# Performance work log

Measured on AMD Instinct MI355X. Metric: run time of the kernel, lower is better.

Reference implementation:

```python
import jax, jax.numpy as jnp
import numpy as np

N, FEAT, NCLS = 8192, 1024, 64


def setup_inputs() -> dict:
    key = jax.random.key(0)
    k1, k2, k3, k4, k5, k6 = jax.random.split(key, 6)
    x = jax.random.normal(k1, (N, FEAT), dtype=jnp.float32)
    adj = jax.random.uniform(k2, (N, N), dtype=jnp.float32)  # pairwise distances
    stdv1 = 1.0 / np.sqrt(FEAT)
    W1 = jax.random.uniform(k3, (FEAT, FEAT), jnp.float32, -stdv1, stdv1)
    b1 = jax.random.uniform(k4, (FEAT,), jnp.float32, -stdv1, stdv1)
    W2 = jax.random.uniform(k5, (FEAT, NCLS), jnp.float32, -stdv1, stdv1)
    b2 = jax.random.uniform(k6, (NCLS,), jnp.float32, -stdv1, stdv1)
    alpha = jnp.full((1,), 0.3, dtype=jnp.float32)
    return {"x": x, "adj": adj, "W1": W1, "b1": b1, "W2": W2, "b2": b2,
            "alpha": alpha, "K": 32}


def reference(x, adj, W1, b1, W2, b2, alpha, K):
    # --- top-K smallest-distance neighbor selection per row ---
    neg_vals, idx = jax.lax.top_k(-adj, K)        # K smallest adj entries per row
    vals = -neg_vals                              # [N, K] distances
    w = jnp.exp(-alpha[0] * vals)                 # 1 / exp(alpha * d)
    w = w / jnp.sum(w, axis=1, keepdims=True)     # row-normalize edge weights

    def spmm(h):
        # sparse A @ h using top-K edge list: out[i] = sum_k w[i,k] * h[idx[i,k]]
        return jnp.einsum('nk,nkf->nf', w, h[idx])

    # 2-layer GCN path of SimTSC (eval mode: dropout is identity)
    h = jax.nn.relu(spmm(x @ W1) + b1)            # [N, FEAT]
    out = spmm(h @ W2) + b2                       # [N, NCLS]
    return jax.nn.log_softmax(out, axis=1)
```

## Files before the change

### kernel.cpp

```cpp
#include <hip/hip_runtime.h>

typedef __bf16 bf16_t;
typedef __bf16 bf16x4 __attribute__((ext_vector_type(4)));
typedef __bf16 bf16x8 __attribute__((ext_vector_type(8)));
typedef float  f32x4  __attribute__((ext_vector_type(4)));

typedef const __attribute__((address_space(1))) void gvoid_t;
typedef __attribute__((address_space(3))) void lvoid_t;

#define N_NODES 8192
#define FEAT    1024
#define NCLS    64
#define TK      32

__device__ __forceinline__ float wave_min_f32(float v) {
  int x = __float_as_int(v), t;
#define STEPF(ctrl) t = __builtin_amdgcn_update_dpp(x, x, ctrl, 0xf, 0xf, false); \
                    v = fminf(v, __int_as_float(t)); x = __float_as_int(v);
  STEPF(0x111)
  STEPF(0x112)
  STEPF(0x114)
  STEPF(0x118)
  STEPF(0x142)
  STEPF(0x143)
#undef STEPF
  return __int_as_float(__builtin_amdgcn_readlane(x, 63));
}

__device__ __forceinline__ unsigned wave_min_u32(unsigned v) {
  int x = (int)v, t;
#define STEPU(ctrl) t = __builtin_amdgcn_update_dpp(x, x, ctrl, 0xf, 0xf, false); \
                    x = (int)((unsigned)x < (unsigned)t ? (unsigned)x : (unsigned)t);
  STEPU(0x111)
  STEPU(0x112)
  STEPU(0x114)
  STEPU(0x118)
  STEPU(0x142)
  STEPU(0x143)
#undef STEPU
  return (unsigned)__builtin_amdgcn_readlane(x, 63);
}

__global__ __launch_bounds__(256) void topk_kernel(const float* __restrict__ adj,
                                                   const float* __restrict__ alphap,
                                                   const float* __restrict__ x,
                                                   bf16_t* __restrict__ x_bf,
                                                   int* __restrict__ idx_out,
                                                   float* __restrict__ w_out,
                                                   const float* __restrict__ W1,
                                                   bf16_t* __restrict__ W1t,
                                                   const float* __restrict__ W2,
                                                   bf16_t* __restrict__ W2t) {
  const int tid = threadIdx.x;
  __shared__ float tile[64][65];
  __shared__ float svals[256];
  __shared__ int   sidx[256];
  __shared__ int   scnt;

  if (blockIdx.x >= N_NODES) {
    const int tb = blockIdx.x - N_NODES;
    const int bxi = tb % 17, by = tb / 17;
    const float* in;
    bf16_t* out;
    int cols, bx;
    if (bxi < 16) { in = W1; out = W1t; cols = FEAT; bx = bxi; }
    else          { in = W2; out = W2t; cols = NCLS; bx = 0; }
#pragma unroll
    for (int i = 0; i < 16; ++i) {
      int li = i * 256 + tid;
      int r = li >> 6, c = li & 63;
      tile[r][c] = in[(size_t)(by * 64 + r) * cols + bx * 64 + c];
    }
    __syncthreads();
#pragma unroll
    for (int i = 0; i < 16; ++i) {
      int li = i * 256 + tid;
      int r = li >> 6, c = li & 63;
      out[(size_t)(bx * 64 + r) * FEAT + by * 64 + c] = (__bf16)tile[c][r];
    }
    return;
  }

  const int row = blockIdx.x;
  {
    const float4 v = ((const float4*)(x + (size_t)row * FEAT))[tid];
    bf16x4 o;
    o[0] = (__bf16)v.x; o[1] = (__bf16)v.y; o[2] = (__bf16)v.z; o[3] = (__bf16)v.w;
    ((bf16x4*)(x_bf + (size_t)row * FEAT))[tid] = o;
  }

  const float* arow = adj + (size_t)row * N_NODES;
  float thr = 1.0f / 128.0f;
  int cnt = 0;
  for (int attempt = 0; attempt < 24; ++attempt) {
    __syncthreads();
    if (tid == 0) scnt = 0;
    __syncthreads();
#pragma unroll
    for (int v = 0; v < 8; ++v) {
      int vi = v * 256 + tid;
      float4 q = ((const float4*)arow)[vi];
      int base = vi * 4;
      if (q.x < thr) { int p = atomicAdd(&scnt, 1); if (p < 256) { svals[p] = q.x; sidx[p] = base;     } }
      if (q.y < thr) { int p = atomicAdd(&scnt, 1); if (p < 256) { svals[p] = q.y; sidx[p] = base + 1; } }
      if (q.z < thr) { int p = atomicAdd(&scnt, 1); if (p < 256) { svals[p] = q.z; sidx[p] = base + 2; } }
      if (q.w < thr) { int p = atomicAdd(&scnt, 1); if (p < 256) { svals[p] = q.w; sidx[p] = base + 3; } }
    }
    __syncthreads();
    cnt = scnt;
    if (cnt >= TK && cnt <= 256) break;
    thr = (cnt < TK) ? thr * 2.0f : thr * 0.5f;
  }
  const int M = cnt < 256 ? cnt : 256;

  if (tid < 64) {
    const int lane = tid;
    const float INF = __int_as_float(0x7f800000);
    float cv[4];
    int   ci[4];
#pragma unroll
    for (int j = 0; j < 4; ++j) {
      int slot = lane + j * 64;
      if (slot < M) { cv[j] = svals[slot]; ci[j] = sidx[slot]; }
      else          { cv[j] = INF;         ci[j] = 0x7fffffff; }
    }
    float selv = 0.f;
    int   seli = 0;
    for (int k = 0; k < TK; ++k) {
      const float lv = fminf(fminf(cv[0], cv[1]), fminf(cv[2], cv[3]));
      const float wv = wave_min_f32(lv);
      unsigned li = 0xffffffffu;
#pragma unroll
      for (int j = 0; j < 4; ++j)
        if (cv[j] == wv) li = li < (unsigned)ci[j] ? li : (unsigned)ci[j];
      const unsigned wi = wave_min_u32(li);
      if (lane == k) { selv = wv; seli = (int)wi; }
#pragma unroll
      for (int j = 0; j < 4; ++j)
        if (cv[j] == wv && (unsigned)ci[j] == wi) cv[j] = INF;
    }
    const float a = alphap[0];
    const float e = (lane < TK) ? expf(-a * selv) : 0.0f;
    float ssum = e;
#pragma unroll
    for (int off = 1; off < 64; off <<= 1) ssum += __shfl_xor(ssum, off);
    if (lane < TK) {
      idx_out[(size_t)row * TK + lane] = seli & (N_NODES - 1);
      w_out[(size_t)row * TK + lane]   = e / ssum;
    }
  }
}

template <int BM, int BN, bool OUT_BF16>
__global__ __launch_bounds__(256, 2) void gemm_bt_kernel(const bf16_t* __restrict__ A,
                                                         const bf16_t* __restrict__ Bt,
                                                         void* __restrict__ Cp,
                                                         int M, int N, int Kd) {
  constexpr int LDSA = BM * 64;
  constexpr int LDSB = BN * 64;
  __shared__ char lds[2][LDSA + LDSB];
  const int tid = threadIdx.x;
  const int wid = tid >> 6, lane = tid & 63;
  const int bm0 = blockIdx.x * BM, bn0 = blockIdx.y * BN;
  const int wr = wid >> 1, wc = wid & 1;
  constexpr int WM = BM / 2, WN = BN / 2;
  constexpr int NMI = WM / 16, NNI = WN / 16;

  auto stage = [&](int buf, int t) {
    const int k0 = t * 32;
#pragma unroll
    for (int li = 0; li < BM / 64; ++li) {
      const int rb = wid * (BM / 4) + li * 16;
      const int r = rb + (lane >> 2);
      const int sdat = (lane & 3) ^ (r & 3);
      const bf16_t* g = A + (size_t)(bm0 + r) * Kd + k0 + sdat * 8;
      __builtin_amdgcn_global_load_lds((gvoid_t*)g, (lvoid_t*)&lds[buf][rb * 64], 16, 0, 0);
    }
#pragma unroll
    for (int li = 0; li < BN / 64; ++li) {
      const int rb = wid * (BN / 4) + li * 16;
      const int r = rb + (lane >> 2);
      const int sdat = (lane & 3) ^ (r & 3);
      const bf16_t* g = Bt + (size_t)(bn0 + r) * Kd + k0 + sdat * 8;
      __builtin_amdgcn_global_load_lds((gvoid_t*)g, (lvoid_t*)&lds[buf][LDSA + rb * 64], 16, 0, 0);
    }
  };

  f32x4 acc[NMI][NNI];
#pragma unroll
  for (int mi = 0; mi < NMI; ++mi)
#pragma unroll
    for (int ni = 0; ni < NNI; ++ni) acc[mi][ni] = (f32x4){0.f, 0.f, 0.f, 0.f};

  const int nT = Kd / 32;
  stage(0, 0);
  __syncthreads();
  for (int t = 0; t < nT; ++t) {
    const int cur = t & 1;
    if (t + 1 < nT) stage(cur ^ 1, t + 1);
    const char* la = &lds[cur][0];
    const char* lb = &lds[cur][LDSA];
    const int s = lane >> 4;
    bf16x8 af[NMI], bfr[NNI];
#pragma unroll
    for (int mi = 0; mi < NMI; ++mi) {
      const int m = wr * WM + mi * 16 + (lane & 15);
      af[mi] = *(const bf16x8*)(la + m * 64 + ((s ^ (m & 3)) * 16));
    }
#pragma unroll
    for (int ni = 0; ni < NNI; ++ni) {
      const int n = wc * WN + ni * 16 + (lane & 15);
      bfr[ni] = *(const bf16x8*)(lb + n * 64 + ((s ^ (n & 3)) * 16));
    }
#pragma unroll
    for (int mi = 0; mi < NMI; ++mi)
#pragma unroll
      for (int ni = 0; ni < NNI; ++ni)
        acc[mi][ni] = __builtin_amdgcn_mfma_f32_16x16x32_bf16(af[mi], bfr[ni], acc[mi][ni], 0, 0, 0);
    __syncthreads();
  }

#pragma unroll
  for (int mi = 0; mi < NMI; ++mi)
#pragma unroll
    for (int ni = 0; ni < NNI; ++ni)
#pragma unroll
      for (int j = 0; j < 4; ++j) {
        const int r = bm0 + wr * WM + mi * 16 + (lane >> 4) * 4 + j;
        const int c = bn0 + wc * WN + ni * 16 + (lane & 15);
        if constexpr (OUT_BF16)
          ((bf16_t*)Cp)[(size_t)r * N + c] = (__bf16)acc[mi][ni][j];
        else
          ((float*)Cp)[(size_t)r * N + c] = acc[mi][ni][j];
      }
}

#define SROWS  16
#define SCHUNK 128
#define NCHUNK 8
__global__ __launch_bounds__(256) void spmm_gemm2_kernel(const bf16_t* __restrict__ xW1,
                                                         const int* __restrict__ idxm,
                                                         const float* __restrict__ wm,
                                                         const float* __restrict__ b1,
                                                         const bf16_t* __restrict__ W2t,
                                                         float* __restrict__ part) {
  const int tid = threadIdx.x;
  const int c  = blockIdx.x & (NCHUNK - 1);
  const int rg = blockIdx.x >> 3;
  const int r0 = rg * SROWS;
  const int f0 = c * SCHUNK;
  __shared__ int    snb[SROWS][TK];
  __shared__ float  swt[SROWS][TK];
  __shared__ bf16_t hls[SROWS][SCHUNK];
  ((int2*)&snb[0][0])[tid]   = ((const int2*)(idxm + (size_t)r0 * TK))[tid];
  ((float2*)&swt[0][0])[tid] = ((const float2*)(wm + (size_t)r0 * TK))[tid];
  __syncthreads();
  const int wid = tid >> 6, lane = tid & 63;
  const int gr = tid >> 4;
  const int gc = (tid & 15) * 8;

  float a[8];
#pragma unroll
  for (int j = 0; j < 8; ++j) a[j] = 0.f;
#pragma unroll 8
  for (int k = 0; k < TK; ++k) {
    const bf16x8 v = *(const bf16x8*)(xW1 + (size_t)snb[gr][k] * FEAT + f0 + gc);
    const float wk = swt[gr][k];
#pragma unroll
    for (int j = 0; j < 8; ++j) a[j] += wk * (float)v[j];
  }
  const float4 b0 = ((const float4*)(b1 + f0 + gc))[0];
  const float4 b1v = ((const float4*)(b1 + f0 + gc))[1];
  bf16x8 o0;
  o0[0] = (__bf16)fmaxf(a[0] + b0.x, 0.f);
  o0[1] = (__bf16)fmaxf(a[1] + b0.y, 0.f);
  o0[2] = (__bf16)fmaxf(a[2] + b0.z, 0.f);
  o0[3] = (__bf16)fmaxf(a[3] + b0.w, 0.f);
  o0[4] = (__bf16)fmaxf(a[4] + b1v.x, 0.f);
  o0[5] = (__bf16)fmaxf(a[5] + b1v.y, 0.f);
  o0[6] = (__bf16)fmaxf(a[6] + b1v.z, 0.f);
  o0[7] = (__bf16)fmaxf(a[7] + b1v.w, 0.f);
  const int g0 = (gc >> 3);
  char* hb = (char*)&hls[0][0];
  *(bf16x8*)(hb + gr * (SCHUNK * 2) + ((g0 ^ (gr & 7)) * 16)) = o0;
  __syncthreads();

  f32x4 acc = (f32x4){0.f, 0.f, 0.f, 0.f};
  const int s = lane >> 4;
  const int m = lane & 15;
  const int n = wid * 16 + (lane & 15);
  const char* hr = (char*)&hls[0][0] + m * (SCHUNK * 2);
#pragma unroll
  for (int ks = 0; ks < SCHUNK / 32; ++ks) {
    const bf16x8 bfrag = *(const bf16x8*)(W2t + (size_t)n * FEAT + f0 + ks * 32 + s * 8);
    const int g = ks * 4 + s;
    const bf16x8 afrag = *(const bf16x8*)(hr + ((g ^ (m & 7)) * 16));
    acc = __builtin_amdgcn_mfma_f32_16x16x32_bf16(afrag, bfrag, acc, 0, 0, 0);
  }
#pragma unroll
  for (int j = 0; j < 4; ++j) {
    const int r = r0 + (lane >> 4) * 4 + j;
    const int col = wid * 16 + (lane & 15);
    part[((size_t)c * N_NODES + r) * NCLS + col] = acc[j];
  }
}

__global__ __launch_bounds__(256) void reduce8_kernel(const float* __restrict__ part,
                                                      float* __restrict__ out2) {
  const int i = blockIdx.x * 256 + threadIdx.x;
  float4 s = ((const float4*)(part))[i];
#pragma unroll
  for (int c = 1; c < NCHUNK; ++c) {
    const float4 p = ((const float4*)(part + (size_t)c * N_NODES * NCLS))[i];
    s.x += p.x; s.y += p.y; s.z += p.z; s.w += p.w;
  }
  ((float4*)out2)[i] = s;
}

__global__ __launch_bounds__(256) void final_kernel(const float* __restrict__ out2,
                                                    const int* __restrict__ idxm,
                                                    const float* __restrict__ wm,
                                                    const float* __restrict__ b2,
                                                    float* __restrict__ out) {
  const int wid = threadIdx.x >> 6, lane = threadIdx.x & 63;
  const int row = blockIdx.x * 4 + wid;
  const int kk = lane & 31;
  const float wv = wm[(size_t)row * TK + kk];
  const int   iv = idxm[(size_t)row * TK + kk];
  float acc = 0.f;
#pragma unroll 8
  for (int k = 0; k < TK; ++k) {
    const float wk = __shfl(wv, k);
    const int   ik = __shfl(iv, k);
    acc += wk * out2[(size_t)ik * NCLS + lane];
  }
  const float logit = acc + b2[lane];
  float m = logit;
#pragma unroll
  for (int off = 1; off < 64; off <<= 1) m = fmaxf(m, __shfl_xor(m, off));
  const float e = expf(logit - m);
  float ssum = e;
#pragma unroll
  for (int off = 1; off < 64; off <<= 1) ssum += __shfl_xor(ssum, off);
  out[(size_t)row * NCLS + lane] = (logit - m) - logf(ssum);
}

extern "C" void kernel_launch(void* const* d_in, const int* in_sizes, int n_in,
                              void* d_out, int out_size, void* d_ws, size_t ws_size,
                              hipStream_t stream) {
  (void)in_sizes; (void)n_in; (void)out_size; (void)ws_size;
  const float* x     = (const float*)d_in[0];
  const float* adj   = (const float*)d_in[1];
  const float* W1    = (const float*)d_in[2];
  const float* b1    = (const float*)d_in[3];
  const float* W2    = (const float*)d_in[4];
  const float* b2    = (const float*)d_in[5];
  const float* alpha = (const float*)d_in[6];

  char* ws = (char*)d_ws;
  const size_t MB = 1024 * 1024;
  bf16_t* x_bf = (bf16_t*)(ws + 0 * MB);
  bf16_t* xW1  = (bf16_t*)(ws + 16 * MB);
  bf16_t* W1t  = (bf16_t*)(ws + 48 * MB);
  bf16_t* W2t  = (bf16_t*)(ws + 50 * MB);
  float*  out2 = (float*)(ws + 51 * MB);
  int*    idxm = (int*)(ws + 53 * MB);
  float*  wm   = (float*)(ws + 54 * MB);
  float*  part = (float*)(ws + 56 * MB);

  topk_kernel<<<dim3(N_NODES + 272), dim3(256), 0, stream>>>(
      adj, alpha, x, x_bf, idxm, wm, W1, W1t, W2, W2t);
  gemm_bt_kernel<128, 128, true><<<dim3(N_NODES / 128, FEAT / 128), dim3(256), 0, stream>>>(
      x_bf, W1t, (void*)xW1, N_NODES, FEAT, FEAT);
  spmm_gemm2_kernel<<<dim3((N_NODES / SROWS) * NCHUNK), dim3(256), 0, stream>>>(
      xW1, idxm, wm, b1, W2t, part);
  reduce8_kernel<<<dim3(N_NODES * NCLS / 4 / 256), dim3(256), 0, stream>>>(part, out2);
  final_kernel<<<dim3(N_NODES / 4), dim3(256), 0, stream>>>(out2, idxm, wm, b2, (float*)d_out);
}
```

Before: 136.1 us.

## Fuse x fp32-to-bf16 conversion into GEMM1 A-tile staging, remap blocks per XCD

Removes the separate x->bf16 conversion from the top-k kernel and instead loads fp32 x directly in the first GEMM, converting to bf16 while writing the swizzled LDS tile. Block indices are remapped so each XCD works on contiguous row tiles, aiming for better L2 locality. In the fused spmm/GEMM2 kernel, W2t fragments are prefetched into registers before the barrier. This saves a 16MB bf16 write and read of x, but A staging now goes through registers as synchronous global loads instead of async global_load_lds, which may stall the GEMM pipeline and doubles A read bytes per tile.

```diff
diff --git a/kernel.cpp b/kernel.cpp
--- a/kernel.cpp
+++ b/kernel.cpp
@@ -43,8 +43,6 @@
 
 __global__ __launch_bounds__(256) void topk_kernel(const float* __restrict__ adj,
                                                    const float* __restrict__ alphap,
-                                                   const float* __restrict__ x,
-                                                   bf16_t* __restrict__ x_bf,
                                                    int* __restrict__ idx_out,
                                                    float* __restrict__ w_out,
                                                    const float* __restrict__ W1,
@@ -82,13 +80,6 @@
   }
 
   const int row = blockIdx.x;
-  {
-    const float4 v = ((const float4*)(x + (size_t)row * FEAT))[tid];
-    bf16x4 o;
-    o[0] = (__bf16)v.x; o[1] = (__bf16)v.y; o[2] = (__bf16)v.z; o[3] = (__bf16)v.w;
-    ((bf16x4*)(x_bf + (size_t)row * FEAT))[tid] = o;
-  }
-
   const float* arow = adj + (size_t)row * N_NODES;
   float thr = 1.0f / 128.0f;
   int cnt = 0;
@@ -151,31 +142,40 @@
   }
 }
 
-template <int BM, int BN, bool OUT_BF16>
-__global__ __launch_bounds__(256, 2) void gemm_bt_kernel(const bf16_t* __restrict__ A,
-                                                         const bf16_t* __restrict__ Bt,
-                                                         void* __restrict__ Cp,
-                                                         int M, int N, int Kd) {
+__global__ __launch_bounds__(256, 2) void gemm1_kernel(const float* __restrict__ A,
+                                                       const bf16_t* __restrict__ Bt,
+                                                       bf16_t* __restrict__ C) {
+  constexpr int BM = 128, BN = 128, Kd = FEAT;
   constexpr int LDSA = BM * 64;
   constexpr int LDSB = BN * 64;
   __shared__ char lds[2][LDSA + LDSB];
   const int tid = threadIdx.x;
   const int wid = tid >> 6, lane = tid & 63;
-  const int bm0 = blockIdx.x * BM, bn0 = blockIdx.y * BN;
+  const int b = blockIdx.x;
+  const int xcd = b & 7, j = b >> 3;
+  const int bm0 = (xcd * 8 + (j >> 3)) * BM;
+  const int bn0 = (j & 7) * BN;
   const int wr = wid >> 1, wc = wid & 1;
   constexpr int WM = BM / 2, WN = BN / 2;
   constexpr int NMI = WM / 16, NNI = WN / 16;
 
-  auto stage = [&](int buf, int t) {
+  auto stageA = [&](int buf, int t) {
     const int k0 = t * 32;
 #pragma unroll
-    for (int li = 0; li < BM / 64; ++li) {
-      const int rb = wid * (BM / 4) + li * 16;
-      const int r = rb + (lane >> 2);
-      const int sdat = (lane & 3) ^ (r & 3);
-      const bf16_t* g = A + (size_t)(bm0 + r) * Kd + k0 + sdat * 8;
-      __builtin_amdgcn_global_load_lds((gvoid_t*)g, (lvoid_t*)&lds[buf][rb * 64], 16, 0, 0);
-    }
+    for (int it = 0; it < 2; ++it) {
+      const int i = it * 256 + tid;
+      const int r = i >> 2, g = i & 3;
+      const float* src = A + (size_t)(bm0 + r) * Kd + k0 + g * 8;
+      const float4 f0 = ((const float4*)src)[0];
+      const float4 f1 = ((const float4*)src)[1];
+      bf16x8 o;
+      o[0] = (__bf16)f0.x; o[1] = (__bf16)f0.y; o[2] = (__bf16)f0.z; o[3] = (__bf16)f0.w;
+      o[4] = (__bf16)f1.x; o[5] = (__bf16)f1.y; o[6] = (__bf16)f1.z; o[7] = (__bf16)f1.w;
+      *(bf16x8*)(&lds[buf][r * 64 + ((g ^ (r & 3)) * 16)]) = o;
+    }
+  };
+  auto stageB = [&](int buf, int t) {
+    const int k0 = t * 32;
 #pragma unroll
     for (int li = 0; li < BN / 64; ++li) {
       const int rb = wid * (BN / 4) + li * 16;
@@ -193,11 +193,12 @@
     for (int ni = 0; ni < NNI; ++ni) acc[mi][ni] = (f32x4){0.f, 0.f, 0.f, 0.f};
 
   const int nT = Kd / 32;
-  stage(0, 0);
+  stageB(0, 0);
+  stageA(0, 0);
   __syncthreads();
   for (int t = 0; t < nT; ++t) {
     const int cur = t & 1;
-    if (t + 1 < nT) stage(cur ^ 1, t + 1);
+    if (t + 1 < nT) { stageB(cur ^ 1, t + 1); stageA(cur ^ 1, t + 1); }
     const char* la = &lds[cur][0];
     const char* lb = &lds[cur][LDSA];
     const int s = lane >> 4;
@@ -225,13 +226,10 @@
 #pragma unroll
     for (int ni = 0; ni < NNI; ++ni)
 #pragma unroll
-      for (int j = 0; j < 4; ++j) {
-        const int r = bm0 + wr * WM + mi * 16 + (lane >> 4) * 4 + j;
+      for (int j4 = 0; j4 < 4; ++j4) {
+        const int r = bm0 + wr * WM + mi * 16 + (lane >> 4) * 4 + j4;
         const int c = bn0 + wc * WN + ni * 16 + (lane & 15);
-        if constexpr (OUT_BF16)
-          ((bf16_t*)Cp)[(size_t)r * N + c] = (__bf16)acc[mi][ni][j];
-        else
-          ((float*)Cp)[(size_t)r * N + c] = acc[mi][ni][j];
+        C[(size_t)r * FEAT + c] = (__bf16)acc[mi][ni][j4];
       }
 }
 
@@ -283,19 +281,23 @@
   const int g0 = (gc >> 3);
   char* hb = (char*)&hls[0][0];
   *(bf16x8*)(hb + gr * (SCHUNK * 2) + ((g0 ^ (gr & 7)) * 16)) = o0;
-  __syncthreads();
-
-  f32x4 acc = (f32x4){0.f, 0.f, 0.f, 0.f};
+
   const int s = lane >> 4;
   const int m = lane & 15;
   const int n = wid * 16 + (lane & 15);
+  bf16x8 bfr[SCHUNK / 32];
+#pragma unroll
+  for (int ks = 0; ks < SCHUNK / 32; ++ks)
+    bfr[ks] = *(const bf16x8*)(W2t + (size_t)n * FEAT + f0 + ks * 32 + s * 8);
+  __syncthreads();
+
+  f32x4 acc = (f32x4){0.f, 0.f, 0.f, 0.f};
   const char* hr = (char*)&hls[0][0] + m * (SCHUNK * 2);
 #pragma unroll
   for (int ks = 0; ks < SCHUNK / 32; ++ks) {
-    const bf16x8 bfrag = *(const bf16x8*)(W2t + (size_t)n * FEAT + f0 + ks * 32 + s * 8);
     const int g = ks * 4 + s;
     const bf16x8 afrag = *(const bf16x8*)(hr + ((g ^ (m & 7)) * 16));
-    acc = __builtin_amdgcn_mfma_f32_16x16x32_bf16(afrag, bfrag, acc, 0, 0, 0);
+    acc = __builtin_amdgcn_mfma_f32_16x16x32_bf16(afrag, bfr[ks], acc, 0, 0, 0);
   }
 #pragma unroll
   for (int j = 0; j < 4; ++j) {
@@ -359,7 +361,6 @@
 
   char* ws = (char*)d_ws;
   const size_t MB = 1024 * 1024;
-  bf16_t* x_bf = (bf16_t*)(ws + 0 * MB);
   bf16_t* xW1  = (bf16_t*)(ws + 16 * MB);
   bf16_t* W1t  = (bf16_t*)(ws + 48 * MB);
   bf16_t* W2t  = (bf16_t*)(ws + 50 * MB);
@@ -369,9 +370,8 @@
   float*  part = (float*)(ws + 56 * MB);
 
   topk_kernel<<<dim3(N_NODES + 272), dim3(256), 0, stream>>>(
-      adj, alpha, x, x_bf, idxm, wm, W1, W1t, W2, W2t);
-  gemm_bt_kernel<128, 128, true><<<dim3(N_NODES / 128, FEAT / 128), dim3(256), 0, stream>>>(
-      x_bf, W1t, (void*)xW1, N_NODES, FEAT, FEAT);
+      adj, alpha, idxm, wm, W1, W1t, W2, W2t);
+  gemm1_kernel<<<dim3(512), dim3(256), 0, stream>>>(x, W1t, xW1);
   spmm_gemm2_kernel<<<dim3((N_NODES / SROWS) * NCHUNK), dim3(256), 0, stream>>>(
       xW1, idxm, wm, b1, W2t, part);
   reduce8_kernel<<<dim3(N_NODES * NCLS / 4 / 256), dim3(256), 0, stream>>>(part, out2);
```

After: 149.0 us. 9.5% more time.
